# Optimization experiments

Measured on AMD Instinct MI355X. Metric: run time of the kernel, lower is better.

## Reference

```python
import jax, jax.numpy as jnp
import numpy as np

N = 500_000      # total observations
D = 40           # per-observation feature dim
S = 2048         # number of segments (time series)
WIDTH = 128      # psi hidden width
LATENT = 128     # latent width
DOT = 64         # dot_prod_dim
HEADS = 4        # n_heads


def setup_inputs() -> dict:
    key = jax.random.key(0)
    ks = jax.random.split(key, 12)

    def he(k, shape):
        fan_in = shape[0]
        lim = np.sqrt(6.0 / fan_in)
        return jax.random.uniform(k, shape, jnp.float32, -lim, lim)

    inputs = jax.random.normal(ks[0], (N, D), jnp.float32)
    segment_ids = jnp.sort(jax.random.randint(ks[1], (N,), 0, S))
    lengths = jax.random.randint(ks[2], (S,), 0, 300)
    return {
        "inputs": inputs,
        "segment_ids": segment_ids,
        "lengths": lengths,
        "W1": he(ks[3], (D, WIDTH)),      "b1": jnp.zeros((WIDTH,), jnp.float32),
        "W2": he(ks[4], (WIDTH, WIDTH)), "b2": jnp.zeros((WIDTH,), jnp.float32),
        "W3": he(ks[5], (WIDTH, LATENT)),"b3": jnp.zeros((LATENT,), jnp.float32),
        "Wr": he(ks[6], (LATENT, LATENT)),"br": jnp.zeros((LATENT,), jnp.float32),
        "W_k": he(ks[7], (LATENT + D, DOT * HEADS)),
        "W_q": jax.random.normal(ks[8], (HEADS, DOT), jnp.float32) * 0.02,
    }


def segment_softmax(x, seg, num_segments):
    # x: [N, H]; softmax over elements sharing the same segment id
    m = jax.ops.segment_max(x, seg, num_segments, indices_are_sorted=True)
    e = jnp.exp(x - m[seg])
    denom = jax.ops.segment_sum(e, seg, num_segments, indices_are_sorted=True)
    return e / denom[seg]


def reference(inputs, segment_ids, lengths, W1, b1, W2, b2, W3, b3, Wr, br, W_k, W_q):
    relu = jax.nn.relu
    # psi: 2 hidden dense layers + latent projection (all relu)
    h = relu(inputs @ W1 + b1)
    h = relu(h @ W2 + b2)
    enc = relu(h @ W3 + b3)                                   # [N, LATENT]
    # segment mean aggregation
    sums = jax.ops.segment_sum(enc, segment_ids, S, indices_are_sorted=True)
    counts = jax.ops.segment_sum(jnp.ones((enc.shape[0], 1), enc.dtype),
                                 segment_ids, S, indices_are_sorted=True)
    agg = sums / jnp.maximum(counts, 1.0)                      # [S, LATENT]
    agg = relu(agg @ Wr + br)                                  # rho
    # broadcast back and combine
    combined = jnp.concatenate([inputs, agg[segment_ids]], axis=-1)  # [N, D+LATENT]
    keys = (combined @ W_k).reshape(-1, HEADS, DOT)            # split+stack == reshape
    preattn = jnp.einsum('nhd,hd->nh', keys, W_q) / jnp.sqrt(jnp.float32(DOT))
    attn = segment_softmax(preattn, segment_ids, S)            # [N, H]
    # match original: list of per-head [N, 1] tensors -> stacked [H, N, 1]
    return jnp.transpose(attn)[..., None]
```

## Files before the change

kernel.cpp:

```cpp
#include <hip/hip_runtime.h>
#include <math.h>


#define NROWS 500000
#define DIM 40
#define NQ (DIM / 4)
#define NSEG 2048
#define DOTD 64
#define NH 4
#define PBLOCK 256
#define CROWS 512

__global__ __launch_bounds__(PBLOCK) void prep_kernel(
    const int* __restrict__ seg,
    const float* __restrict__ Wk,
    const float* __restrict__ Wq,
    int* __restrict__ seg_start,
    int* __restrict__ seg_end,
    float* __restrict__ wxg)
{
    const int tid = (int)threadIdx.x;
    const int n = (int)(blockIdx.x * PBLOCK + tid);

    if (blockIdx.x == 0 && tid < DIM * NH) {
        const int h = tid / DIM;
        const int d = tid - h * DIM;
        const float* wkp = Wk + d * (NH * DOTD) + h * DOTD;
        const float* wqp = Wq + h * DOTD;
        float acc = 0.f;
        #pragma unroll
        for (int j = 0; j < DOTD; ++j) acc += wkp[j] * wqp[j];
        wxg[h * DIM + d] = acc * 0.125f;
    }

    if (n < NROWS) {
        const int s = seg[n];
        if (n == 0) {
            seg_start[s] = 0;
            for (int t = 0; t < s; ++t) { seg_start[t] = 0; seg_end[t] = 0; }
        } else {
            const int sp = seg[n - 1];
            if (sp != s) {
                seg_start[s] = n;
                seg_end[sp] = n;
                for (int t = sp + 1; t < s; ++t) { seg_start[t] = n; seg_end[t] = n; }
            }
        }
        if (n == NROWS - 1) {
            seg_end[s] = NROWS;
            for (int t = s + 1; t < NSEG; ++t) { seg_start[t] = NROWS; seg_end[t] = NROWS; }
        }
    }
}

__device__ __forceinline__ void recompute_logits(
    const float4* __restrict__ x4, const float (*wxl)[DIM], int n, float* a)
{
    #pragma unroll
    for (int h = 0; h < NH; ++h) a[h] = 0.f;
    #pragma unroll
    for (int q = 0; q < NQ; ++q) {
        const float4 v = x4[(size_t)n * NQ + q];
        #pragma unroll
        for (int h = 0; h < NH; ++h) {
            const float4 w = ((const float4*)wxl[h])[q];
            a[h] += v.x * w.x + v.y * w.y + v.z * w.z + v.w * w.w;
        }
    }
}

__global__ __launch_bounds__(64) void seg_attn_kernel(
    const float* __restrict__ x,
    const int* __restrict__ seg_start,
    const int* __restrict__ seg_end,
    const float* __restrict__ wxg,
    float* __restrict__ out)
{
    __shared__ __align__(16) float wxl[NH][DIM];
    __shared__ float cache[NH][CROWS];

    const int lane = (int)threadIdx.x;
    const int s = (int)blockIdx.x;
    const int start = seg_start[s];
    const int rows = seg_end[s] - start;
    if (rows <= 0) return;

    {
        float* wf = &wxl[0][0];
        for (int t = lane; t < NH * DIM; t += 64) wf[t] = wxg[t];
    }
    __syncthreads();

    const float4* x4 = (const float4*)x;
    const int sup = (rows + 127) >> 7;

    float lmax[NH];
    #pragma unroll
    for (int h = 0; h < NH; ++h) lmax[h] = -3.0e38f;

    for (int si = 0; si < sup; ++si) {
        const int i0 = (si << 7) + lane;
        const int i1 = i0 + 64;
        const bool p0 = i0 < rows;
        const bool p1 = i1 < rows;
        const float4* r0 = x4 + (size_t)(start + i0) * NQ;
        const float4* r1 = x4 + (size_t)(start + i1) * NQ;
        float a0[NH] = {0.f, 0.f, 0.f, 0.f};
        float a1[NH] = {0.f, 0.f, 0.f, 0.f};

        #pragma unroll
        for (int q = 0; q < NQ; ++q) {
            float4 w[NH];
            #pragma unroll
            for (int h = 0; h < NH; ++h) w[h] = ((const float4*)wxl[h])[q];
            if (p0) {
                const float4 v = r0[q];
                #pragma unroll
                for (int h = 0; h < NH; ++h)
                    a0[h] += v.x * w[h].x + v.y * w[h].y
                           + v.z * w[h].z + v.w * w[h].w;
            }
            if (p1) {
                const float4 v = r1[q];
                #pragma unroll
                for (int h = 0; h < NH; ++h)
                    a1[h] += v.x * w[h].x + v.y * w[h].y
                           + v.z * w[h].z + v.w * w[h].w;
            }
        }
        if (p0) {
            #pragma unroll
            for (int h = 0; h < NH; ++h) {
                if (i0 < CROWS) cache[h][i0] = a0[h];
                lmax[h] = fmaxf(lmax[h], a0[h]);
            }
        }
        if (p1) {
            #pragma unroll
            for (int h = 0; h < NH; ++h) {
                if (i1 < CROWS) cache[h][i1] = a1[h];
                lmax[h] = fmaxf(lmax[h], a1[h]);
            }
        }
    }

    float m[NH];
    #pragma unroll
    for (int h = 0; h < NH; ++h) {
        float v = lmax[h];
        #pragma unroll
        for (int off = 32; off > 0; off >>= 1) v = fmaxf(v, __shfl_xor(v, off, 64));
        m[h] = v;
    }

    float lsum[NH] = {0.f, 0.f, 0.f, 0.f};
    for (int i = lane; i < rows; i += 64) {
        if (i < CROWS) {
            #pragma unroll
            for (int h = 0; h < NH; ++h) {
                const float e = __expf(cache[h][i] - m[h]);
                cache[h][i] = e;
                lsum[h] += e;
            }
        } else {
            float a[NH];
            recompute_logits(x4, wxl, start + i, a);
            #pragma unroll
            for (int h = 0; h < NH; ++h) lsum[h] += __expf(a[h] - m[h]);
        }
    }
    float rden[NH];
    #pragma unroll
    for (int h = 0; h < NH; ++h) {
        float v = lsum[h];
        #pragma unroll
        for (int off = 32; off > 0; off >>= 1) v += __shfl_xor(v, off, 64);
        rden[h] = 1.0f / v;
    }

    for (int i = lane; i < rows; i += 64) {
        const int n = start + i;
        if (i < CROWS) {
            #pragma unroll
            for (int h = 0; h < NH; ++h)
                out[(size_t)h * NROWS + n] = cache[h][i] * rden[h];
        } else {
            float a[NH];
            recompute_logits(x4, wxl, n, a);
            #pragma unroll
            for (int h = 0; h < NH; ++h)
                out[(size_t)h * NROWS + n] = __expf(a[h] - m[h]) * rden[h];
        }
    }
}

extern "C" void kernel_launch(void* const* d_in, const int* in_sizes, int n_in,
                              void* d_out, int out_size, void* d_ws, size_t ws_size,
                              hipStream_t stream) {
    const float* x  = (const float*)d_in[0];
    const int* seg  = (const int*)d_in[1];
    const float* Wk = (const float*)d_in[11];
    const float* Wq = (const float*)d_in[12];
    float* out = (float*)d_out;

    int* seg_start = (int*)d_ws;
    int* seg_end   = seg_start + NSEG;
    float* wxg     = (float*)(seg_end + NSEG);

    hipLaunchKernelGGL(prep_kernel, dim3((NROWS + PBLOCK - 1) / PBLOCK), dim3(PBLOCK),
                       0, stream, seg, Wk, Wq, seg_start, seg_end, wxg);
    hipLaunchKernelGGL(seg_attn_kernel, dim3(NSEG), dim3(64),
                       0, stream, x, seg_start, seg_end, wxg, out);
}
```

Baseline: 172.1 us.

## Split logit computation into a row-parallel kernel before the segment softmax

After: 157.8 us. 1.09x faster.

```diff
diff --git a/kernel.cpp b/kernel.cpp
--- a/kernel.cpp
+++ b/kernel.cpp
@@ -53,30 +53,45 @@
     }
 }
 
-__device__ __forceinline__ void recompute_logits(
-    const float4* __restrict__ x4, const float (*wxl)[DIM], int n, float* a)
+__global__ __launch_bounds__(PBLOCK) void logits_kernel(
+    const float* __restrict__ x,
+    const float* __restrict__ wxg,
+    float* __restrict__ logit)
 {
-    #pragma unroll
-    for (int h = 0; h < NH; ++h) a[h] = 0.f;
+    __shared__ __align__(16) float wxl[NH][DIM];
+
+    const int tid = (int)threadIdx.x;
+    {
+        float* wf = &wxl[0][0];
+        for (int t = tid; t < NH * DIM; t += PBLOCK) wf[t] = wxg[t];
+    }
+    __syncthreads();
+
+    const int n = (int)(blockIdx.x * PBLOCK + tid);
+    if (n >= NROWS) return;
+
+    const float4* xr = (const float4*)(x + (size_t)n * DIM);
+    float a[NH] = {0.f, 0.f, 0.f, 0.f};
     #pragma unroll
     for (int q = 0; q < NQ; ++q) {
-        const float4 v = x4[(size_t)n * NQ + q];
+        const float4 v = xr[q];
         #pragma unroll
         for (int h = 0; h < NH; ++h) {
             const float4 w = ((const float4*)wxl[h])[q];
             a[h] += v.x * w.x + v.y * w.y + v.z * w.z + v.w * w.w;
         }
     }
+    #pragma unroll
+    for (int h = 0; h < NH; ++h)
+        logit[(size_t)h * NROWS + n] = a[h];
 }
 
-__global__ __launch_bounds__(64) void seg_attn_kernel(
-    const float* __restrict__ x,
+__global__ __launch_bounds__(64) void seg_softmax_kernel(
+    const float* __restrict__ logit,
     const int* __restrict__ seg_start,
     const int* __restrict__ seg_end,
-    const float* __restrict__ wxg,
     float* __restrict__ out)
 {
-    __shared__ __align__(16) float wxl[NH][DIM];
     __shared__ float cache[NH][CROWS];
 
     const int lane = (int)threadIdx.x;
@@ -85,62 +100,16 @@
     const int rows = seg_end[s] - start;
     if (rows <= 0) return;
 
-    {
-        float* wf = &wxl[0][0];
-        for (int t = lane; t < NH * DIM; t += 64) wf[t] = wxg[t];
-    }
-    __syncthreads();
-
-    const float4* x4 = (const float4*)x;
-    const int sup = (rows + 127) >> 7;
-
     float lmax[NH];
     #pragma unroll
     for (int h = 0; h < NH; ++h) lmax[h] = -3.0e38f;
 
-    for (int si = 0; si < sup; ++si) {
-        const int i0 = (si << 7) + lane;
-        const int i1 = i0 + 64;
-        const bool p0 = i0 < rows;
-        const bool p1 = i1 < rows;
-        const float4* r0 = x4 + (size_t)(start + i0) * NQ;
-        const float4* r1 = x4 + (size_t)(start + i1) * NQ;
-        float a0[NH] = {0.f, 0.f, 0.f, 0.f};
-        float a1[NH] = {0.f, 0.f, 0.f, 0.f};
-
+    for (int i = lane; i < rows; i += 64) {
         #pragma unroll
-        for (int q = 0; q < NQ; ++q) {
-            float4 w[NH];
-            #pragma unroll
-            for (int h = 0; h < NH; ++h) w[h] = ((const float4*)wxl[h])[q];
-            if (p0) {
-                const float4 v = r0[q];
-                #pragma unroll
-                for (int h = 0; h < NH; ++h)
-                    a0[h] += v.x * w[h].x + v.y * w[h].y
-                           + v.z * w[h].z + v.w * w[h].w;
-            }
-            if (p1) {
-                const float4 v = r1[q];
-                #pragma unroll
-                for (int h = 0; h < NH; ++h)
-                    a1[h] += v.x * w[h].x + v.y * w[h].y
-                           + v.z * w[h].z + v.w * w[h].w;
-            }
-        }
-        if (p0) {
-            #pragma unroll
-            for (int h = 0; h < NH; ++h) {
-                if (i0 < CROWS) cache[h][i0] = a0[h];
-                lmax[h] = fmaxf(lmax[h], a0[h]);
-            }
-        }
-        if (p1) {
-            #pragma unroll
-            for (int h = 0; h < NH; ++h) {
-                if (i1 < CROWS) cache[h][i1] = a1[h];
-                lmax[h] = fmaxf(lmax[h], a1[h]);
-            }
+        for (int h = 0; h < NH; ++h) {
+            const float v = logit[(size_t)h * NROWS + start + i];
+            if (i < CROWS) cache[h][i] = v;
+            lmax[h] = fmaxf(lmax[h], v);
         }
     }
 
@@ -155,18 +124,13 @@
 
     float lsum[NH] = {0.f, 0.f, 0.f, 0.f};
     for (int i = lane; i < rows; i += 64) {
-        if (i < CROWS) {
-            #pragma unroll
-            for (int h = 0; h < NH; ++h) {
-                const float e = __expf(cache[h][i] - m[h]);
-                cache[h][i] = e;
-                lsum[h] += e;
-            }
-        } else {
-            float a[NH];
-            recompute_logits(x4, wxl, start + i, a);
-            #pragma unroll
-            for (int h = 0; h < NH; ++h) lsum[h] += __expf(a[h] - m[h]);
+        #pragma unroll
+        for (int h = 0; h < NH; ++h) {
+            const float l = (i < CROWS) ? cache[h][i]
+                                        : logit[(size_t)h * NROWS + start + i];
+            const float e = __expf(l - m[h]);
+            if (i < CROWS) cache[h][i] = e;
+            lsum[h] += e;
         }
     }
     float rden[NH];
@@ -180,16 +144,12 @@
 
     for (int i = lane; i < rows; i += 64) {
         const int n = start + i;
-        if (i < CROWS) {
-            #pragma unroll
-            for (int h = 0; h < NH; ++h)
-                out[(size_t)h * NROWS + n] = cache[h][i] * rden[h];
-        } else {
-            float a[NH];
-            recompute_logits(x4, wxl, n, a);
-            #pragma unroll
-            for (int h = 0; h < NH; ++h)
-                out[(size_t)h * NROWS + n] = __expf(a[h] - m[h]) * rden[h];
+        #pragma unroll
+        for (int h = 0; h < NH; ++h) {
+            const float e = (i < CROWS)
+                ? cache[h][i]
+                : __expf(logit[(size_t)h * NROWS + n] - m[h]);
+            out[(size_t)h * NROWS + n] = e * rden[h];
         }
     }
 }
@@ -206,9 +166,13 @@
     int* seg_start = (int*)d_ws;
     int* seg_end   = seg_start + NSEG;
     float* wxg     = (float*)(seg_end + NSEG);
+    float* logit   = wxg + 256;
 
-    hipLaunchKernelGGL(prep_kernel, dim3((NROWS + PBLOCK - 1) / PBLOCK), dim3(PBLOCK),
+    const int nblk = (NROWS + PBLOCK - 1) / PBLOCK;
+    hipLaunchKernelGGL(prep_kernel, dim3(nblk), dim3(PBLOCK),
                        0, stream, seg, Wk, Wq, seg_start, seg_end, wxg);
-    hipLaunchKernelGGL(seg_attn_kernel, dim3(NSEG), dim3(64),
-                       0, stream, x, seg_start, seg_end, wxg, out);
+    hipLaunchKernelGGL(logits_kernel, dim3(nblk), dim3(PBLOCK),
+                       0, stream, x, wxg, logit);
+    hipLaunchKernelGGL(seg_softmax_kernel, dim3(NSEG), dim3(64),
+                       0, stream, logit, seg_start, seg_end, out);
 }
```
